# Kernel tuning notes

Measured on AMD Instinct MI355X. Metric: run time of the kernel, lower is better.

The kernel has to match this reference:

```python
import jax, jax.numpy as jnp
import numpy as np

BATCH = 131072
N = 64          # total bits
PARTS = 16      # len(partition) == dpp_size
M = 4           # bits per part
D = PARTS
EPS = 1e-8


def _colnorm(a):
    return a / jnp.linalg.norm(a, axis=0, keepdims=True)


def setup_inputs() -> dict:
    key = jax.random.key(0)
    k0, k1, k2, k3, k4 = jax.random.split(key, 5)
    x = jax.random.randint(k0, (BATCH, N), 0, 2, dtype=jnp.int32)
    W = jax.random.normal(k1, (PARTS, (1 << M) - 1), dtype=jnp.float32)
    A = _colnorm(jax.random.normal(k2, (D, D), dtype=jnp.float32))
    B = _colnorm(jax.random.normal(k3, (D, D), dtype=jnp.float32))
    C = _colnorm(jax.random.normal(k4, (D, D), dtype=jnp.float32))
    return {"x": x, "W": W, "A": A, "B": B, "C": C}


def reference(x, W, A, B, C):
    batch = x.shape[0]
    # --- Simple PCs (vectorized over the 16 parts): bit-pack each 4-bit part ---
    bits = x.reshape(batch, PARTS, M)                       # contiguous partition
    pow2 = (1 << jnp.arange(M)).astype(jnp.int32)           # [M]
    idx = jnp.sum(bits * pow2, axis=-1)                     # [B, P] in [0, 2^M)
    w = jax.nn.softmax(W, axis=-1)                          # [P, 2^M - 1]
    w = jnp.concatenate([jnp.zeros((PARTS, 1), w.dtype), w], axis=-1)  # [P, 2^M]
    p = w[jnp.arange(PARTS)[None, :], idx]                  # [B, P]

    # --- L matrix: sym PD part + skew part ---
    I = jnp.eye(D, dtype=A.dtype)
    L0 = A.T @ A + (B @ C.T - C @ B.T) + EPS * I            # [D, D]

    # column-scale by p, then force diagonal to 1 where p == 0
    Lp = L0[None, :, :] * p[:, None, :]                     # [B, D, D]
    eye_b = jnp.eye(D, dtype=bool)
    mask = eye_b[None, :, :] & (p == 0.0)[:, :, None]
    Lp = jnp.where(mask, jnp.asarray(1.0, Lp.dtype), Lp)

    sign, logabs = jnp.linalg.slogdet(Lp)                   # [B]
    y = logabs + jnp.log(jax.lax.stop_gradient(sign))       # nan if det < 0 (matches torch.logdet)
    s0, la0 = jnp.linalg.slogdet(L0 + I)
    alpha = la0 + jnp.log(jax.lax.stop_gradient(s0))
    return y - alpha
```

## Files before the change

kernel.cpp:

```cpp
#include <hip/hip_runtime.h>
#include <math.h>

#define BATCH 131072
#define EPS 1e-8f
#define OVF_CAP 16384u


__global__ __launch_bounds__(256) void prep_kernel(
    const float* __restrict__ W, const float* __restrict__ A,
    const float* __restrict__ Bm, const float* __restrict__ Cm,
    float* __restrict__ ws) {
    __shared__ float sAug[16 * 34];
    __shared__ float sLI[16 * 17];
    int t = threadIdx.x;
    int i = t >> 4, j = t & 15;

    float s = 0.f;
    #pragma unroll
    for (int k = 0; k < 16; ++k) {
        s += A[k * 16 + i] * A[k * 16 + j];
        s += Bm[i * 16 + k] * Cm[j * 16 + k]
           - Cm[i * 16 + k] * Bm[j * 16 + k];
    }
    if (i == j) s += EPS;
    sAug[i * 34 + j] = s;
    sAug[i * 34 + 16 + j] = (i == j) ? 1.f : 0.f;
    sLI[i * 17 + j] = s + ((i == j) ? 1.f : 0.f);
    __syncthreads();

    float logdetAcc = 0.f, alphaAcc = 0.f;
    for (int k = 0; k < 16; ++k) {
        float piv  = sAug[k * 34 + k];
        float f    = sAug[i * 34 + k];
        float pivL = sLI[k * 17 + k];
        float g    = sLI[i * 17 + k];
        logdetAcc += __logf(fabsf(piv));
        alphaAcc  += __logf(fabsf(pivL));
        __syncthreads();
        if (t < 32) sAug[k * 34 + t] *= 1.f / piv;
        __syncthreads();
        if (i != k) {
            sAug[i * 34 + j]      = fmaf(-f, sAug[k * 34 + j],      sAug[i * 34 + j]);
            sAug[i * 34 + 16 + j] = fmaf(-f, sAug[k * 34 + 16 + j], sAug[i * 34 + 16 + j]);
        }
        if (i > k) {
            sLI[i * 17 + j] = fmaf(-g / pivL, sLI[k * 17 + j], sLI[i * 17 + j]);
        }
        __syncthreads();
    }

    ws[272 + i * 16 + j] = sAug[i * 34 + 16 + j];
    if (t == 0) { ws[528] = logdetAcc; ws[529] = alphaAcc; }
    if (t == 17) ((unsigned*)ws)[530] = 0u;
    if (t == 18) ws[271] = 0.f;

    if (t < 16) {
        float row[15];
        float mx = -1e30f;
        #pragma unroll
        for (int q = 0; q < 15; ++q) { row[q] = W[t * 15 + q]; mx = fmaxf(mx, row[q]); }
        float se = 0.f;
        #pragma unroll
        for (int q = 0; q < 15; ++q) se += expf(row[q] - mx);
        float lse = mx + logf(se);
        ws[t * 17 + 0] = 0.f;
        #pragma unroll
        for (int q = 0; q < 15; ++q) ws[t * 17 + 1 + q] = row[q] - lse;
    }
}

__global__ __launch_bounds__(256) void main_kernel(const int4* __restrict__ x4,
                                                   float* __restrict__ ws,
                                                   float* __restrict__ out) {
    __shared__ float sLW[272];
    __shared__ float sM[272];
    int t = threadIdx.x;
    sLW[t] = ws[t];
    if (t < 16) sLW[256 + t] = ws[256 + t];
    sM[(t >> 4) * 17 + (t & 15)] = ws[272 + t];
    __syncthreads();

    int l = t & 15;
    int grp = t >> 4;
    int b = blockIdx.x * 16 + grp;

    int4 v = x4[(size_t)blockIdx.x * 256 + t];
    int idx = v.x + 2 * v.y + 4 * v.z + 8 * v.w;
    float lw = sLW[l * 17 + idx];

    unsigned lane = t & 63;
    unsigned long long wmask = __ballot(idx != 0);
    unsigned gm = (unsigned)((wmask >> (lane & 48)) & 0xFFFFull);

    lw += __shfl_xor(lw, 1);
    lw += __shfl_xor(lw, 2);
    lw += __shfl_xor(lw, 4);
    lw += __shfl_xor(lw, 8);

    if (l == 0) {
        unsigned zb = (~gm) & 0xFFFFu;
        int z = __popc(zb);
        float base = lw + ws[528] - ws[529];
        if (z <= 5) {
            int zi[5];
            unsigned tt = zb;
            #pragma unroll
            for (int q = 0; q < 5; ++q) {
                zi[q] = tt ? (__ffs(tt) - 1) : 0;
                tt &= tt - 1;
            }
            float m[5][5];
            #pragma unroll
            for (int r = 0; r < 5; ++r)
                #pragma unroll
                for (int c = 0; c < 5; ++c)
                    m[r][c] = (r < z && c < z) ? sM[zi[r] * 17 + zi[c]]
                                               : ((r == c) ? 1.f : 0.f);
            float logd = 0.f;
            #pragma unroll
            for (int k = 0; k < 5; ++k) {
                float piv = m[k][k];
                logd += __logf(fabsf(piv));
                float inv = 1.0f / piv;
                #pragma unroll
                for (int r = k + 1; r < 5; ++r) {
                    float f = m[r][k] * inv;
                    #pragma unroll
                    for (int c = k + 1; c < 5; ++c)
                        m[r][c] = fmaf(-f, m[k][c], m[r][c]);
                }
            }
            out[b] = base + logd;
        } else {
            unsigned pos = atomicAdd(((unsigned*)ws) + 530, 1u);
            if (pos < OVF_CAP) {
                ((int*)ws)[544 + 2 * pos] = b;
                ((int*)ws)[545 + 2 * pos] = (int)zb;
            }
            out[b] = base;
        }
    }
}

__global__ __launch_bounds__(64, 1) void cleanup_kernel(const float* __restrict__ ws,
                                                        float* __restrict__ out) {
    __shared__ float sM[256];
    int lt = threadIdx.x;
    #pragma unroll
    for (int q = 0; q < 4; ++q) sM[lt * 4 + q] = ws[272 + lt * 4 + q];
    __syncthreads();

    unsigned n = ((const unsigned*)ws)[530];
    if (n > OVF_CAP) n = OVF_CAP;
    unsigned stride = 8u * 64u;
    for (unsigned ii = blockIdx.x * 64u + (unsigned)lt; ii < n; ii += stride) {
        int b = ((const int*)ws)[544 + 2 * ii];
        unsigned Z = (unsigned)((const int*)ws)[545 + 2 * ii];

        float a[16][16];
        #pragma unroll
        for (int j = 0; j < 16; ++j) {
            bool on = (Z >> j) & 1u;
            #pragma unroll
            for (int i = 0; i < 16; ++i) {
                float v2 = on ? sM[i * 16 + j] : 0.f;
                if (i == j && !on) v2 = 1.f;
                a[i][j] = v2;
            }
        }
        float logdet = 0.f;
        #pragma unroll
        for (int k = 0; k < 16; ++k) {
            float piv = a[k][k];
            logdet += __logf(fabsf(piv));
            float inv = 1.0f / piv;
            #pragma unroll
            for (int i2 = k + 1; i2 < 16; ++i2) {
                float f = a[i2][k] * inv;
                #pragma unroll
                for (int j2 = k + 1; j2 < 16; ++j2)
                    a[i2][j2] = fmaf(-f, a[k][j2], a[i2][j2]);
            }
        }
        out[b] += logdet;
    }
}

extern "C" void kernel_launch(void* const* d_in, const int* in_sizes, int n_in,
                              void* d_out, int out_size, void* d_ws, size_t ws_size,
                              hipStream_t stream) {
    const int4*  x = (const int4*)d_in[0];
    const float* W = (const float*)d_in[1];
    const float* A = (const float*)d_in[2];
    const float* B = (const float*)d_in[3];
    const float* C = (const float*)d_in[4];
    float* ws  = (float*)d_ws;
    float* out = (float*)d_out;

    prep_kernel<<<1, 256, 0, stream>>>(W, A, B, C, ws);
    main_kernel<<<BATCH / 16, 256, 0, stream>>>(x, ws, out);
    cleanup_kernel<<<8, 64, 0, stream>>>(ws, out);
}
```

Measured before the change: 105.7 us.

## Use register LU in prep kernel and compact small-det work into one wave

```diff
diff --git a/kernel.cpp b/kernel.cpp
--- a/kernel.cpp
+++ b/kernel.cpp
@@ -6,85 +6,115 @@
 #define OVF_CAP 16384u
 
 
-__global__ __launch_bounds__(256) void prep_kernel(
+__global__ __launch_bounds__(64, 1) void prep_kernel(
     const float* __restrict__ W, const float* __restrict__ A,
     const float* __restrict__ Bm, const float* __restrict__ Cm,
     float* __restrict__ ws) {
-    __shared__ float sAug[16 * 34];
-    __shared__ float sLI[16 * 17];
+    __shared__ float sL0[256];
     int t = threadIdx.x;
-    int i = t >> 4, j = t & 15;
-
-    float s = 0.f;
+
+    #pragma unroll
+    for (int q = 0; q < 4; ++q) {
+        int e = t * 4 + q, i = e >> 4, j = e & 15;
+        float s = 0.f;
+        #pragma unroll
+        for (int k = 0; k < 16; ++k) {
+            s += A[k * 16 + i] * A[k * 16 + j];
+            s += Bm[i * 16 + k] * Cm[j * 16 + k]
+               - Cm[i * 16 + k] * Bm[j * 16 + k];
+        }
+        if (i == j) s += EPS;
+        sL0[e] = s;
+    }
+    __syncthreads();
+
+    float dAdd = (t >= 16 && t < 32) ? 1.f : 0.f;
+    float a[16][16];
+    #pragma unroll
+    for (int i = 0; i < 16; ++i)
+        #pragma unroll
+        for (int j = 0; j < 16; ++j)
+            a[i][j] = sL0[i * 16 + j] + ((i == j) ? dAdd : 0.f);
+
+    float logdet = 0.f;
     #pragma unroll
     for (int k = 0; k < 16; ++k) {
-        s += A[k * 16 + i] * A[k * 16 + j];
-        s += Bm[i * 16 + k] * Cm[j * 16 + k]
-           - Cm[i * 16 + k] * Bm[j * 16 + k];
-    }
-    if (i == j) s += EPS;
-    sAug[i * 34 + j] = s;
-    sAug[i * 34 + 16 + j] = (i == j) ? 1.f : 0.f;
-    sLI[i * 17 + j] = s + ((i == j) ? 1.f : 0.f);
-    __syncthreads();
-
-    float logdetAcc = 0.f, alphaAcc = 0.f;
-    for (int k = 0; k < 16; ++k) {
-        float piv  = sAug[k * 34 + k];
-        float f    = sAug[i * 34 + k];
-        float pivL = sLI[k * 17 + k];
-        float g    = sLI[i * 17 + k];
-        logdetAcc += __logf(fabsf(piv));
-        alphaAcc  += __logf(fabsf(pivL));
-        __syncthreads();
-        if (t < 32) sAug[k * 34 + t] *= 1.f / piv;
-        __syncthreads();
-        if (i != k) {
-            sAug[i * 34 + j]      = fmaf(-f, sAug[k * 34 + j],      sAug[i * 34 + j]);
-            sAug[i * 34 + 16 + j] = fmaf(-f, sAug[k * 34 + 16 + j], sAug[i * 34 + 16 + j]);
-        }
-        if (i > k) {
-            sLI[i * 17 + j] = fmaf(-g / pivL, sLI[k * 17 + j], sLI[i * 17 + j]);
-        }
-        __syncthreads();
-    }
-
-    ws[272 + i * 16 + j] = sAug[i * 34 + 16 + j];
-    if (t == 0) { ws[528] = logdetAcc; ws[529] = alphaAcc; }
-    if (t == 17) ((unsigned*)ws)[530] = 0u;
-    if (t == 18) ws[271] = 0.f;
+        float piv = a[k][k];
+        logdet += __logf(fabsf(piv));
+        float inv = 1.0f / piv;
+        #pragma unroll
+        for (int i2 = k + 1; i2 < 16; ++i2) {
+            float f = a[i2][k] * inv;
+            a[i2][k] = f;
+            #pragma unroll
+            for (int j2 = k + 1; j2 < 16; ++j2)
+                a[i2][j2] = fmaf(-f, a[k][j2], a[i2][j2]);
+        }
+    }
+    if (t == 0)  ws[528] = logdet;
+    if (t == 16) ws[529] = logdet;
 
     if (t < 16) {
+        int c = t;
+        float y[16];
+        #pragma unroll
+        for (int i = 0; i < 16; ++i) {
+            float v = (i == c) ? 1.f : 0.f;
+            #pragma unroll
+            for (int k = 0; k < 16; ++k)
+                if (k < i) v = fmaf(-a[i][k], y[k], v);
+            y[i] = v;
+        }
+        float xc[16];
+        #pragma unroll
+        for (int i = 15; i >= 0; --i) {
+            float v = y[i];
+            #pragma unroll
+            for (int k = 0; k < 16; ++k)
+                if (k > i) v = fmaf(-a[i][k], xc[k], v);
+            xc[i] = v / a[i][i];
+        }
+        #pragma unroll
+        for (int i = 0; i < 16; ++i) ws[272 + i * 16 + c] = xc[i];
+    }
+
+    if (t >= 32 && t < 48) {
+        int r = t - 32;
         float row[15];
         float mx = -1e30f;
         #pragma unroll
-        for (int q = 0; q < 15; ++q) { row[q] = W[t * 15 + q]; mx = fmaxf(mx, row[q]); }
+        for (int q = 0; q < 15; ++q) { row[q] = W[r * 15 + q]; mx = fmaxf(mx, row[q]); }
         float se = 0.f;
         #pragma unroll
         for (int q = 0; q < 15; ++q) se += expf(row[q] - mx);
         float lse = mx + logf(se);
-        ws[t * 17 + 0] = 0.f;
-        #pragma unroll
-        for (int q = 0; q < 15; ++q) ws[t * 17 + 1 + q] = row[q] - lse;
-    }
-}
-
-__global__ __launch_bounds__(256) void main_kernel(const int4* __restrict__ x4,
-                                                   float* __restrict__ ws,
-                                                   float* __restrict__ out) {
+        ws[r * 17 + 0] = 0.f;
+        #pragma unroll
+        for (int q = 0; q < 15; ++q) ws[r * 17 + 1 + q] = row[q] - lse;
+    }
+    if (t == 48) ((unsigned*)ws)[530] = 0u;
+    if (t == 49) ws[271] = 0.f;
+}
+
+__global__ __launch_bounds__(1024) void main_kernel(const int4* __restrict__ x4,
+                                                    float* __restrict__ ws,
+                                                    float* __restrict__ out) {
     __shared__ float sLW[272];
     __shared__ float sM[272];
+    __shared__ float sLw[64];
+    __shared__ unsigned sGm[64];
     int t = threadIdx.x;
-    sLW[t] = ws[t];
-    if (t < 16) sLW[256 + t] = ws[256 + t];
-    sM[(t >> 4) * 17 + (t & 15)] = ws[272 + t];
+    if (t < 272) sLW[t] = ws[t];
+    else if (t >= 288 && t < 544) {
+        int u = t - 288;
+        sM[(u >> 4) * 17 + (u & 15)] = ws[272 + u];
+    }
     __syncthreads();
 
     int l = t & 15;
-    int grp = t >> 4;
-    int b = blockIdx.x * 16 + grp;
-
-    int4 v = x4[(size_t)blockIdx.x * 256 + t];
+    int g = t >> 4;
+
+    int4 v = x4[(size_t)blockIdx.x * 1024 + t];
     int idx = v.x + 2 * v.y + 4 * v.z + 8 * v.w;
     float lw = sLW[l * 17 + idx];
 
@@ -97,10 +127,14 @@
     lw += __shfl_xor(lw, 4);
     lw += __shfl_xor(lw, 8);
 
-    if (l == 0) {
-        unsigned zb = (~gm) & 0xFFFFu;
+    if (l == 0) { sLw[g] = lw; sGm[g] = gm; }
+    __syncthreads();
+
+    if (t < 64) {
+        int b = blockIdx.x * 64 + t;
+        unsigned zb = (~sGm[t]) & 0xFFFFu;
         int z = __popc(zb);
-        float base = lw + ws[528] - ws[529];
+        float base = sLw[t] + ws[528] - ws[529];
         if (z <= 5) {
             int zi[5];
             unsigned tt = zb;
@@ -197,7 +231,7 @@
     float* ws  = (float*)d_ws;
     float* out = (float*)d_out;
 
-    prep_kernel<<<1, 256, 0, stream>>>(W, A, B, C, ws);
-    main_kernel<<<BATCH / 16, 256, 0, stream>>>(x, ws, out);
+    prep_kernel<<<1, 64, 0, stream>>>(W, A, B, C, ws);
+    main_kernel<<<BATCH / 64, 1024, 0, stream>>>(x, ws, out);
     cleanup_kernel<<<8, 64, 0, stream>>>(ws, out);
 }
```

Measured after the change: 100.9 us. -4.5%, faster.
